# Kernel tuning notes

Hardware: AMD Instinct MI355X
Metric: run time of the kernel (lower is better)

Reference implementation:

```python
import jax, jax.numpy as jnp
import numpy as np

D_MODEL = 1024
NUM_HEADS = 16
HEAD_DIM = D_MODEL // NUM_HEADS


def setup_inputs() -> dict:
    key = jax.random.key(0)
    ks = jax.random.split(key, 9)
    s = 1.0 / np.sqrt(D_MODEL)
    x = jax.random.normal(ks[0], (2, 2048, D_MODEL), dtype=jnp.float32)
    Wq = jax.random.normal(ks[1], (D_MODEL, D_MODEL), dtype=jnp.float32) * s
    bq = jnp.zeros((D_MODEL,), dtype=jnp.float32)
    Wk = jax.random.normal(ks[2], (D_MODEL, D_MODEL), dtype=jnp.float32) * s
    bk = jnp.zeros((D_MODEL,), dtype=jnp.float32)
    Wv = jax.random.normal(ks[3], (D_MODEL, D_MODEL), dtype=jnp.float32) * s
    bv = jnp.zeros((D_MODEL,), dtype=jnp.float32)
    Wo = jax.random.normal(ks[4], (D_MODEL, D_MODEL), dtype=jnp.float32) * s
    bo = jnp.zeros((D_MODEL,), dtype=jnp.float32)
    return {"x": x, "Wq": Wq, "bq": bq, "Wk": Wk, "bk": bk,
            "Wv": Wv, "bv": bv, "Wo": Wo, "bo": bo}


def reference(x, Wq, bq, Wk, bk, Wv, bv, Wo, bo):
    B, S, D = x.shape
    H, Hd = NUM_HEADS, HEAD_DIM
    scale = 1.0 / np.sqrt(Hd)

    def split_heads(t):  # [B,S,D] -> [B,H,S,Hd]
        return t.reshape(B, S, H, Hd).transpose(0, 2, 1, 3)

    q = split_heads(x @ Wq + bq)
    k = split_heads(x @ Wk + bk)
    v = split_heads(x @ Wv + bv)

    scores = jnp.einsum('bhqd,bhkd->bhqk', q, k) * scale
    scores = scores - jnp.max(scores, axis=-1, keepdims=True)
    attn = jax.nn.softmax(scores, axis=-1)
    attended = jnp.einsum('bhqk,bhkd->bhqd', attn, v)
    attended = attended.transpose(0, 2, 1, 3).reshape(B, S, D)
    return attended @ Wo + bo
```

## Files before the change

### kernel.cpp

```cpp
#include <hip/hip_runtime.h>
#include <hip/hip_bf16.h>

typedef __bf16 bf16_t;
typedef __bf16 bf16x8 __attribute__((ext_vector_type(8)));
typedef __bf16 bf16x4 __attribute__((ext_vector_type(4)));
typedef float floatx4 __attribute__((ext_vector_type(4)));
typedef short short4v __attribute__((ext_vector_type(4)));

#define D_MODEL 1024
#define SEQ     2048
#define BATCH   2
#define NHEAD   16
#define HDIM    64
#define MTOT    (BATCH * SEQ)
#define LROWS   (32 * 2048)
#define OPS     (32 * 64 * 2048)

#define QSCALE  0.18033688011112042f

union PBu { bf16x4 b; short4v s; };

__device__ __forceinline__ void async_copy16(const bf16_t* g, bf16_t* l) {
    __builtin_amdgcn_global_load_lds(
        (const __attribute__((address_space(1))) void*)g,
        (__attribute__((address_space(3))) void*)l, 16, 0, 0);
}

__global__ void cvt_f32_bf16(const float* __restrict__ x, bf16_t* __restrict__ y, int n) {
    int i = (blockIdx.x * 256 + threadIdx.x) * 4;
    if (i < n) {
        const float4 v = *(const float4*)(x + i);
        bf16x4 o = { (bf16_t)v.x, (bf16_t)v.y, (bf16_t)v.z, (bf16_t)v.w };
        *(bf16x4*)(y + i) = o;
    }
}

__global__ void transpose_w4(
    const float* __restrict__ W0, const float* __restrict__ W1,
    const float* __restrict__ W2, const float* __restrict__ W3,
    bf16_t* __restrict__ T0, bf16_t* __restrict__ T1,
    bf16_t* __restrict__ T2, bf16_t* __restrict__ T3)
{
    __shared__ float tile[32][33];
    const int z = blockIdx.z;
    const float* W = (z == 0) ? W0 : (z == 1) ? W1 : (z == 2) ? W2 : W3;
    bf16_t*     Wt = (z == 0) ? T0 : (z == 1) ? T1 : (z == 2) ? T2 : T3;
    const int tx = threadIdx.x, ty = threadIdx.y;
    const int k0 = blockIdx.y * 32, n0 = blockIdx.x * 32;
#pragma unroll
    for (int j = 0; j < 32; j += 8)
        tile[ty + j][tx] = W[(size_t)(k0 + ty + j) * D_MODEL + n0 + tx];
    __syncthreads();
#pragma unroll
    for (int j = 0; j < 32; j += 8)
        Wt[(size_t)(n0 + ty + j) * D_MODEL + k0 + tx] = (bf16_t)tile[tx][ty + j];
}

__device__ __forceinline__ void gemm_mainloop(
    const bf16_t* __restrict__ A, const bf16_t* __restrict__ Bt,
    int m0, int n0, bf16_t* As, bf16_t* Bs, floatx4 acc[4][4])
{
    const int tid  = threadIdx.x;
    const int lane = tid & 63;
    const int wid  = tid >> 6;
    const int quad = lane >> 4;
    const int col  = lane & 15;
    const int wm   = (wid >> 1) * 64;
    const int wn   = (wid & 1) * 64;
    const int srow = tid >> 3;
    const int scc  = ((tid & 7) ^ (srow & 7)) * 8;
    const int xorc = col & 7;

    const bf16_t* Ag = A  + (size_t)(m0 + srow) * D_MODEL + scc;
    const bf16_t* Bg = Bt + (size_t)(n0 + srow) * D_MODEL + scc;
    bf16_t* Al = As + tid * 8;
    bf16_t* Bl = Bs + tid * 8;

    for (int kb = 0; kb < D_MODEL; kb += 64) {
#pragma unroll
        for (int p = 0; p < 4; ++p) {
            async_copy16(Ag + kb + p * (32 * D_MODEL), Al + p * 2048);
            async_copy16(Bg + kb + p * (32 * D_MODEL), Bl + p * 2048);
        }
        __syncthreads();
#pragma unroll
        for (int kh = 0; kh < 2; ++kh) {
            bf16x8 af[4], bfr[4];
#pragma unroll
            for (int i = 0; i < 4; ++i)
                af[i] = *(const bf16x8*)(As + (wm + i * 16 + col) * 64 + (((kh * 4 + quad) ^ xorc) * 8));
#pragma unroll
            for (int j = 0; j < 4; ++j)
                bfr[j] = *(const bf16x8*)(Bs + (wn + j * 16 + col) * 64 + (((kh * 4 + quad) ^ xorc) * 8));
#pragma unroll
            for (int i = 0; i < 4; ++i)
#pragma unroll
                for (int j = 0; j < 4; ++j)
                    acc[i][j] = __builtin_amdgcn_mfma_f32_16x16x32_bf16(af[i], bfr[j], acc[i][j], 0, 0, 0);
        }
        __syncthreads();
    }
}

__global__ __launch_bounds__(256, 2) void gemm_qkv(
    const bf16_t* __restrict__ xb,
    const bf16_t* __restrict__ Wtq, const bf16_t* __restrict__ Wtk, const bf16_t* __restrict__ Wtv,
    const float* __restrict__ bq, const float* __restrict__ bk, const float* __restrict__ bv,
    bf16_t* __restrict__ Q, bf16_t* __restrict__ Kh, bf16_t* __restrict__ Vt)
{
    __shared__ bf16_t As[128 * 64];
    __shared__ bf16_t Bs[128 * 64];
    const int z = blockIdx.z;
    const bf16_t* Bt   = (z == 0) ? Wtq : (z == 1) ? Wtk : Wtv;
    const float*  bias = (z == 0) ? bq  : (z == 1) ? bk  : bv;
    bf16_t*       O    = (z == 0) ? Q   : (z == 1) ? Kh  : Vt;
    const float   qs   = (z == 0) ? QSCALE : 1.0f;
    const int m0 = blockIdx.y * 128;
    const int n0 = blockIdx.x * 128;

    floatx4 acc[4][4];
#pragma unroll
    for (int i = 0; i < 4; ++i)
#pragma unroll
        for (int j = 0; j < 4; ++j)
            acc[i][j] = (floatx4){0.f, 0.f, 0.f, 0.f};

    gemm_mainloop(xb, Bt, m0, n0, As, Bs, acc);

    const int tid  = threadIdx.x;
    const int lane = tid & 63;
    const int wid  = tid >> 6;
    const int quad = lane >> 4;
    const int col  = lane & 15;
    const int wm   = (wid >> 1) * 64;
    const int wn   = (wid & 1) * 64;

    if (z == 2) {
#pragma unroll
        for (int i = 0; i < 4; ++i) {
#pragma unroll
            for (int j = 0; j < 4; ++j) {
                const int n = n0 + wn + j * 16 + col;
                const float bb = bias[n];
                const int mb = m0 + wm + i * 16 + quad * 4;
                const size_t bhb = (size_t)((mb >> 11) * NHEAD + (n >> 6)) * (SEQ * HDIM);
                bf16x4 pk = { (bf16_t)(acc[i][j][0] + bb), (bf16_t)(acc[i][j][1] + bb),
                              (bf16_t)(acc[i][j][2] + bb), (bf16_t)(acc[i][j][3] + bb) };
                *(bf16x4*)(O + bhb + (size_t)(n & 63) * SEQ + (mb & 2047)) = pk;
            }
        }
    } else {
#pragma unroll
        for (int i = 0; i < 4; ++i) {
#pragma unroll
            for (int j = 0; j < 4; ++j) {
                const int n = n0 + wn + j * 16 + col;
                const float bb = bias[n];
#pragma unroll
                for (int r = 0; r < 4; ++r) {
                    const int m = m0 + wm + i * 16 + quad * 4 + r;
                    const float v = (acc[i][j][r] + bb) * qs;
                    const size_t bhb = (size_t)((m >> 11) * NHEAD + (n >> 6)) * (SEQ * HDIM);
                    O[bhb + (size_t)(m & 2047) * HDIM + (n & 63)] = (bf16_t)v;
                }
            }
        }
    }
}

__global__ __launch_bounds__(256, 3) void attn_kernel(
    const bf16_t* __restrict__ Q, const bf16_t* __restrict__ K,
    const bf16_t* __restrict__ Vt, float* __restrict__ Opart, float* __restrict__ lpart)
{
    __shared__ bf16_t Ks[64 * 64];
    __shared__ bf16_t Vs[64 * 64];

    const int tid  = threadIdx.x;
    const int lane = tid & 63;
    const int wid  = tid >> 6;
    const int quad = lane >> 4;
    const int col  = lane & 15;
    const int xorc = col & 7;
    const int bh   = blockIdx.y;
    const int sp   = blockIdx.z;
    const int q0   = blockIdx.x * 128;
    const int srow = tid >> 3;
    const int scc  = ((tid & 7) ^ (srow & 7)) * 8;

    const bf16_t* Qb = Q  + (size_t)bh * (SEQ * HDIM);
    const bf16_t* Kb = K  + (size_t)bh * (SEQ * HDIM);
    const bf16_t* Vb = Vt + (size_t)bh * (SEQ * HDIM);

    bf16x8 qf[2][2];
#pragma unroll
    for (int st = 0; st < 2; ++st) {
        const int qrow = q0 + wid * 32 + st * 16 + col;
        qf[st][0] = *(const bf16x8*)(Qb + (size_t)qrow * HDIM + quad * 8);
        qf[st][1] = *(const bf16x8*)(Qb + (size_t)qrow * HDIM + 32 + quad * 8);
    }

    floatx4 o_acc[2][4];
    float lsum[2] = {0.f, 0.f};
#pragma unroll
    for (int st = 0; st < 2; ++st)
#pragma unroll
        for (int dt = 0; dt < 4; ++dt)
            o_acc[st][dt] = (floatx4){0.f, 0.f, 0.f, 0.f};

    const bf16_t* Kg = Kb + (size_t)(sp * 1024 + srow) * HDIM + scc;
    const bf16_t* Vg = Vb + (size_t)srow * SEQ + sp * 1024 + scc;
    bf16_t* KsL = Ks + tid * 8;
    bf16_t* VsL = Vs + tid * 8;

    for (int it = 0; it < 16; ++it) {
        const int ko = it * 64;
        async_copy16(Kg + (size_t)ko * HDIM, KsL);
        async_copy16(Kg + (size_t)(ko + 32) * HDIM, KsL + 2048);
        async_copy16(Vg + ko, VsL);
        async_copy16(Vg + (size_t)32 * SEQ + ko, VsL + 2048);
        __syncthreads();

        bf16x8 kf[4][2];
#pragma unroll
        for (int t = 0; t < 4; ++t) {
            kf[t][0] = *(const bf16x8*)(Ks + (t * 16 + col) * 64 + ((quad ^ xorc) * 8));
            kf[t][1] = *(const bf16x8*)(Ks + (t * 16 + col) * 64 + (((4 + quad) ^ xorc) * 8));
        }
        short4v vfr[4][4];
#pragma unroll
        for (int dt = 0; dt < 4; ++dt)
#pragma unroll
            for (int t = 0; t < 4; ++t) {
                const int sch = t * 2 + (quad >> 1);
                vfr[dt][t] = *(const short4v*)(Vs + (dt * 16 + col) * 64 + ((sch ^ xorc) * 8) + (quad & 1) * 4);
            }

#pragma unroll
        for (int st = 0; st < 2; ++st) {
            floatx4 s_acc[4];
            short4v pb[4];
#pragma unroll
            for (int t = 0; t < 4; ++t) {
                s_acc[t] = (floatx4){0.f, 0.f, 0.f, 0.f};
                s_acc[t] = __builtin_amdgcn_mfma_f32_16x16x32_bf16(kf[t][0], qf[st][0], s_acc[t], 0, 0, 0);
                s_acc[t] = __builtin_amdgcn_mfma_f32_16x16x32_bf16(kf[t][1], qf[st][1], s_acc[t], 0, 0, 0);
            }
#pragma unroll
            for (int t = 0; t < 4; ++t) {
                const float p0 = exp2f(s_acc[t][0]);
                const float p1 = exp2f(s_acc[t][1]);
                const float p2 = exp2f(s_acc[t][2]);
                const float p3 = exp2f(s_acc[t][3]);
                lsum[st] += (p0 + p1) + (p2 + p3);
                PBu u;
                u.b = (bf16x4){ (bf16_t)p0, (bf16_t)p1, (bf16_t)p2, (bf16_t)p3 };
                pb[t] = u.s;
            }
#pragma unroll
            for (int dt = 0; dt < 4; ++dt)
#pragma unroll
                for (int t = 0; t < 4; ++t)
                    o_acc[st][dt] = __builtin_amdgcn_mfma_f32_16x16x16bf16_1k(vfr[dt][t], pb[t], o_acc[st][dt], 0, 0, 0);
        }
        __syncthreads();
    }

#pragma unroll
    for (int st = 0; st < 2; ++st) {
        lsum[st] += __shfl_xor(lsum[st], 16, 64);
        lsum[st] += __shfl_xor(lsum[st], 32, 64);
    }

    const size_t osp = (size_t)sp * OPS + (size_t)bh * 64 * 2048;
#pragma unroll
    for (int st = 0; st < 2; ++st) {
        const int q = q0 + wid * 32 + st * 16 + col;
#pragma unroll
        for (int dt = 0; dt < 4; ++dt)
#pragma unroll
            for (int r = 0; r < 4; ++r) {
                const int d = dt * 16 + quad * 4 + r;
                Opart[osp + (size_t)d * 2048 + q] = o_acc[st][dt][r];
            }
        if (lane < 16)
            lpart[(size_t)sp * LROWS + (size_t)bh * 2048 + q0 + wid * 32 + st * 16 + lane] = lsum[st];
    }
}

__global__ __launch_bounds__(256) void attn_combine(
    const float* __restrict__ Op, const float* __restrict__ lp, bf16_t* __restrict__ A2)
{
    __shared__ float Linv[64];
    __shared__ bf16_t T[64 * 72];
    const int tid = threadIdx.x;
    const int qb  = blockIdx.x * 64;
    const int bh  = blockIdx.y;
    const int b   = bh >> 4, h = bh & 15;

    if (tid < 64)
        Linv[tid] = 1.0f / (lp[(size_t)bh * 2048 + qb + tid] + lp[LROWS + (size_t)bh * 2048 + qb + tid]);
    __syncthreads();

    const int d  = tid >> 2;
    const int qo = (tid & 3) * 16;
    const size_t base = ((size_t)bh * 64 + d) * 2048 + qb + qo;
#pragma unroll
    for (int i = 0; i < 16; i += 4) {
        const float4 a = *(const float4*)(Op + base + i);
        const float4 c = *(const float4*)(Op + OPS + base + i);
        T[(qo + i + 0) * 72 + d] = (bf16_t)((a.x + c.x) * Linv[qo + i + 0]);
        T[(qo + i + 1) * 72 + d] = (bf16_t)((a.y + c.y) * Linv[qo + i + 1]);
        T[(qo + i + 2) * 72 + d] = (bf16_t)((a.z + c.z) * Linv[qo + i + 2]);
        T[(qo + i + 3) * 72 + d] = (bf16_t)((a.w + c.w) * Linv[qo + i + 3]);
    }
    __syncthreads();

    const int q  = tid >> 2;
    const int dd = (tid & 3) * 16;
    const bf16x8 o0 = *(const bf16x8*)(T + q * 72 + dd);
    const bf16x8 o1 = *(const bf16x8*)(T + q * 72 + dd + 8);
    bf16_t* dst = A2 + ((size_t)(b * 2048 + qb + q)) * D_MODEL + h * 64 + dd;
    *(bf16x8*)(dst) = o0;
    *(bf16x8*)(dst + 8) = o1;
}

__global__ __launch_bounds__(256, 2) void gemm_proj(
    const bf16_t* __restrict__ A2, const bf16_t* __restrict__ Wto,
    const float* __restrict__ bo, float* __restrict__ out)
{
    __shared__ bf16_t As[128 * 64];
    __shared__ bf16_t Bs[128 * 64];
    const int m0 = blockIdx.y * 128;
    const int n0 = blockIdx.x * 128;

    floatx4 acc[4][4];
#pragma unroll
    for (int i = 0; i < 4; ++i)
#pragma unroll
        for (int j = 0; j < 4; ++j)
            acc[i][j] = (floatx4){0.f, 0.f, 0.f, 0.f};

    gemm_mainloop(A2, Wto, m0, n0, As, Bs, acc);

    const int tid  = threadIdx.x;
    const int lane = tid & 63;
    const int wid  = tid >> 6;
    const int quad = lane >> 4;
    const int col  = lane & 15;
    const int wm   = (wid >> 1) * 64;
    const int wn   = (wid & 1) * 64;

#pragma unroll
    for (int i = 0; i < 4; ++i) {
#pragma unroll
        for (int j = 0; j < 4; ++j) {
            const int n = n0 + wn + j * 16 + col;
            const float bb = bo[n];
#pragma unroll
            for (int r = 0; r < 4; ++r) {
                const int m = m0 + wm + i * 16 + quad * 4 + r;
                out[(size_t)m * D_MODEL + n] = acc[i][j][r] + bb;
            }
        }
    }
}

extern "C" void kernel_launch(void* const* d_in, const int* in_sizes, int n_in,
                              void* d_out, int out_size, void* d_ws, size_t ws_size,
                              hipStream_t stream) {
    const float* x  = (const float*)d_in[0];
    const float* Wq = (const float*)d_in[1];
    const float* bq = (const float*)d_in[2];
    const float* Wk = (const float*)d_in[3];
    const float* bk = (const float*)d_in[4];
    const float* Wv = (const float*)d_in[5];
    const float* bv = (const float*)d_in[6];
    const float* Wo = (const float*)d_in[7];
    const float* bo = (const float*)d_in[8];
    float* out = (float*)d_out;

    const size_t MB = 1ull << 20;
    char* ws = (char*)d_ws;
    bf16_t* Q     = (bf16_t*)(ws + 0 * MB);
    bf16_t* Kh    = (bf16_t*)(ws + 8 * MB);
    bf16_t* Vt    = (bf16_t*)(ws + 16 * MB);
    bf16_t* A2    = (bf16_t*)(ws + 24 * MB);
    bf16_t* xb    = (bf16_t*)(ws + 32 * MB);
    float*  lpart = (float*)(ws + 32 * MB);
    bf16_t* Wtq   = (bf16_t*)(ws + 40 * MB);
    bf16_t* Wtk   = (bf16_t*)(ws + 42 * MB);
    bf16_t* Wtv   = (bf16_t*)(ws + 44 * MB);
    bf16_t* Wto   = (bf16_t*)(ws + 46 * MB);
    float*  Opart = (float*)(ws + 48 * MB);

    const int nx = MTOT * D_MODEL;
    cvt_f32_bf16<<<nx / (256 * 4), 256, 0, stream>>>(x, xb, nx);

    transpose_w4<<<dim3(D_MODEL / 32, D_MODEL / 32, 4), dim3(32, 8), 0, stream>>>(
        Wq, Wk, Wv, Wo, Wtq, Wtk, Wtv, Wto);

    gemm_qkv<<<dim3(D_MODEL / 128, MTOT / 128, 3), 256, 0, stream>>>(
        xb, Wtq, Wtk, Wtv, bq, bk, bv, Q, Kh, Vt);

    attn_kernel<<<dim3(SEQ / 128, BATCH * NHEAD, 2), 256, 0, stream>>>(
        Q, Kh, Vt, Opart, lpart);

    attn_combine<<<dim3(SEQ / 64, BATCH * NHEAD), 256, 0, stream>>>(Opart, lpart, A2);

    gemm_proj<<<dim3(D_MODEL / 128, MTOT / 128), 256, 0, stream>>>(A2, Wto, bo, out);
}
```

Baseline: 210.4 us.

## Enlarge attention KV tile to 128, shrink proj GEMM M tile, raise occupancy

The attention kernel now stages 128 keys and values per iteration instead of 64. That halves the number of loop iterations and barriers, at the cost of twice the LDS per block, while the occupancy hint rises to 4. The output projection GEMM moves to 64x128 tiles with its own inlined main loop, doubling the grid size so more blocks cover the CUs. Occupancy hints on the QKV and projection GEMMs are also raised to 3, which may force register pressure or spills.

```diff
diff --git a/kernel.cpp b/kernel.cpp
--- a/kernel.cpp
+++ b/kernel.cpp
@@ -102,7 +102,7 @@
     }
 }
 
-__global__ __launch_bounds__(256, 2) void gemm_qkv(
+__global__ __launch_bounds__(256, 3) void gemm_qkv(
     const bf16_t* __restrict__ xb,
     const bf16_t* __restrict__ Wtq, const bf16_t* __restrict__ Wtk, const bf16_t* __restrict__ Wtv,
     const float* __restrict__ bq, const float* __restrict__ bk, const float* __restrict__ bv,
@@ -168,12 +168,12 @@
     }
 }
 
-__global__ __launch_bounds__(256, 3) void attn_kernel(
+__global__ __launch_bounds__(256, 4) void attn_kernel(
     const bf16_t* __restrict__ Q, const bf16_t* __restrict__ K,
     const bf16_t* __restrict__ Vt, float* __restrict__ Opart, float* __restrict__ lpart)
 {
-    __shared__ bf16_t Ks[64 * 64];
-    __shared__ bf16_t Vs[64 * 64];
+    __shared__ bf16_t Ks[128 * 64];
+    __shared__ bf16_t Vs[64 * 128];
 
     const int tid  = threadIdx.x;
     const int lane = tid & 63;
@@ -184,8 +184,6 @@
     const int bh   = blockIdx.y;
     const int sp   = blockIdx.z;
     const int q0   = blockIdx.x * 128;
-    const int srow = tid >> 3;
-    const int scc  = ((tid & 7) ^ (srow & 7)) * 8;
 
     const bf16_t* Qb = Q  + (size_t)bh * (SEQ * HDIM);
     const bf16_t* Kb = K  + (size_t)bh * (SEQ * HDIM);
@@ -207,60 +205,68 @@
         for (int dt = 0; dt < 4; ++dt)
             o_acc[st][dt] = (floatx4){0.f, 0.f, 0.f, 0.f};
 
-    const bf16_t* Kg = Kb + (size_t)(sp * 1024 + srow) * HDIM + scc;
-    const bf16_t* Vg = Vb + (size_t)srow * SEQ + sp * 1024 + scc;
+    const int krow = tid >> 3;
+    const int sccK = ((tid & 7) ^ (krow & 7)) * 8;
+    const int vrow = tid >> 4;
+    const int sccV = ((tid & 15) ^ (vrow & 7)) * 8;
+    const bf16_t* Kg = Kb + (size_t)(sp * 1024 + krow) * HDIM + sccK;
+    const bf16_t* Vg = Vb + (size_t)vrow * SEQ + sp * 1024 + sccV;
     bf16_t* KsL = Ks + tid * 8;
     bf16_t* VsL = Vs + tid * 8;
 
-    for (int it = 0; it < 16; ++it) {
-        const int ko = it * 64;
-        async_copy16(Kg + (size_t)ko * HDIM, KsL);
-        async_copy16(Kg + (size_t)(ko + 32) * HDIM, KsL + 2048);
-        async_copy16(Vg + ko, VsL);
-        async_copy16(Vg + (size_t)32 * SEQ + ko, VsL + 2048);
-        __syncthreads();
-
-        bf16x8 kf[4][2];
-#pragma unroll
-        for (int t = 0; t < 4; ++t) {
-            kf[t][0] = *(const bf16x8*)(Ks + (t * 16 + col) * 64 + ((quad ^ xorc) * 8));
-            kf[t][1] = *(const bf16x8*)(Ks + (t * 16 + col) * 64 + (((4 + quad) ^ xorc) * 8));
-        }
-        short4v vfr[4][4];
-#pragma unroll
-        for (int dt = 0; dt < 4; ++dt)
+    for (int it = 0; it < 8; ++it) {
+        const int ko = it * 128;
+#pragma unroll
+        for (int p = 0; p < 4; ++p) {
+            async_copy16(Kg + (size_t)(ko + p * 32) * HDIM, KsL + p * 2048);
+            async_copy16(Vg + ko + (size_t)(p * 16) * SEQ, VsL + p * 2048);
+        }
+        __syncthreads();
+
+#pragma unroll
+        for (int kh = 0; kh < 2; ++kh) {
+            bf16x8 kf[4][2];
 #pragma unroll
             for (int t = 0; t < 4; ++t) {
-                const int sch = t * 2 + (quad >> 1);
-                vfr[dt][t] = *(const short4v*)(Vs + (dt * 16 + col) * 64 + ((sch ^ xorc) * 8) + (quad & 1) * 4);
-            }
-
-#pragma unroll
-        for (int st = 0; st < 2; ++st) {
-            floatx4 s_acc[4];
-            short4v pb[4];
-#pragma unroll
-            for (int t = 0; t < 4; ++t) {
-                s_acc[t] = (floatx4){0.f, 0.f, 0.f, 0.f};
-                s_acc[t] = __builtin_amdgcn_mfma_f32_16x16x32_bf16(kf[t][0], qf[st][0], s_acc[t], 0, 0, 0);
-                s_acc[t] = __builtin_amdgcn_mfma_f32_16x16x32_bf16(kf[t][1], qf[st][1], s_acc[t], 0, 0, 0);
-            }
-#pragma unroll
-            for (int t = 0; t < 4; ++t) {
-                const float p0 = exp2f(s_acc[t][0]);
-                const float p1 = exp2f(s_acc[t][1]);
-                const float p2 = exp2f(s_acc[t][2]);
-                const float p3 = exp2f(s_acc[t][3]);
-                lsum[st] += (p0 + p1) + (p2 + p3);
-                PBu u;
-                u.b = (bf16x4){ (bf16_t)p0, (bf16_t)p1, (bf16_t)p2, (bf16_t)p3 };
-                pb[t] = u.s;
-            }
+                kf[t][0] = *(const bf16x8*)(Ks + (kh * 64 + t * 16 + col) * 64 + ((quad ^ xorc) * 8));
+                kf[t][1] = *(const bf16x8*)(Ks + (kh * 64 + t * 16 + col) * 64 + (((4 + quad) ^ xorc) * 8));
+            }
+            short4v vfr[4][4];
 #pragma unroll
             for (int dt = 0; dt < 4; ++dt)
 #pragma unroll
-                for (int t = 0; t < 4; ++t)
-                    o_acc[st][dt] = __builtin_amdgcn_mfma_f32_16x16x16bf16_1k(vfr[dt][t], pb[t], o_acc[st][dt], 0, 0, 0);
+                for (int t = 0; t < 4; ++t) {
+                    const int sch = kh * 8 + t * 2 + (quad >> 1);
+                    vfr[dt][t] = *(const short4v*)(Vs + (dt * 16 + col) * 128 + ((sch ^ xorc) * 8) + (quad & 1) * 4);
+                }
+
+#pragma unroll
+            for (int st = 0; st < 2; ++st) {
+                floatx4 s_acc[4];
+                short4v pb[4];
+#pragma unroll
+                for (int t = 0; t < 4; ++t) {
+                    s_acc[t] = (floatx4){0.f, 0.f, 0.f, 0.f};
+                    s_acc[t] = __builtin_amdgcn_mfma_f32_16x16x32_bf16(kf[t][0], qf[st][0], s_acc[t], 0, 0, 0);
+                    s_acc[t] = __builtin_amdgcn_mfma_f32_16x16x32_bf16(kf[t][1], qf[st][1], s_acc[t], 0, 0, 0);
+                }
+#pragma unroll
+                for (int t = 0; t < 4; ++t) {
+                    const float p0 = exp2f(s_acc[t][0]);
+                    const float p1 = exp2f(s_acc[t][1]);
+                    const float p2 = exp2f(s_acc[t][2]);
+                    const float p3 = exp2f(s_acc[t][3]);
+                    lsum[st] += (p0 + p1) + (p2 + p3);
+                    PBu u;
+                    u.b = (bf16x4){ (bf16_t)p0, (bf16_t)p1, (bf16_t)p2, (bf16_t)p3 };
+                    pb[t] = u.s;
+                }
+#pragma unroll
+                for (int dt = 0; dt < 4; ++dt)
+#pragma unroll
+                    for (int t = 0; t < 4; ++t)
+                        o_acc[st][dt] = __builtin_amdgcn_mfma_f32_16x16x16bf16_1k(vfr[dt][t], pb[t], o_acc[st][dt], 0, 0, 0);
+            }
         }
         __syncthreads();
     }
@@ -324,34 +330,66 @@
     *(bf16x8*)(dst + 8) = o1;
 }
 
-__global__ __launch_bounds__(256, 2) void gemm_proj(
+__global__ __launch_bounds__(256, 3) void gemm_proj(
     const bf16_t* __restrict__ A2, const bf16_t* __restrict__ Wto,
     const float* __restrict__ bo, float* __restrict__ out)
 {
-    __shared__ bf16_t As[128 * 64];
+    __shared__ bf16_t As[64 * 64];
     __shared__ bf16_t Bs[128 * 64];
-    const int m0 = blockIdx.y * 128;
+    const int m0 = blockIdx.y * 64;
     const int n0 = blockIdx.x * 128;
-
-    floatx4 acc[4][4];
-#pragma unroll
-    for (int i = 0; i < 4; ++i)
-#pragma unroll
-        for (int j = 0; j < 4; ++j)
-            acc[i][j] = (floatx4){0.f, 0.f, 0.f, 0.f};
-
-    gemm_mainloop(A2, Wto, m0, n0, As, Bs, acc);
 
     const int tid  = threadIdx.x;
     const int lane = tid & 63;
     const int wid  = tid >> 6;
     const int quad = lane >> 4;
     const int col  = lane & 15;
-    const int wm   = (wid >> 1) * 64;
+    const int wm   = (wid >> 1) * 32;
     const int wn   = (wid & 1) * 64;
-
-#pragma unroll
-    for (int i = 0; i < 4; ++i) {
+    const int srow = tid >> 3;
+    const int scc  = ((tid & 7) ^ (srow & 7)) * 8;
+    const int xorc = col & 7;
+
+    floatx4 acc[2][4];
+#pragma unroll
+    for (int i = 0; i < 2; ++i)
+#pragma unroll
+        for (int j = 0; j < 4; ++j)
+            acc[i][j] = (floatx4){0.f, 0.f, 0.f, 0.f};
+
+    const bf16_t* Ag = A2  + (size_t)(m0 + srow) * D_MODEL + scc;
+    const bf16_t* Bg = Wto + (size_t)(n0 + srow) * D_MODEL + scc;
+    bf16_t* Al = As + tid * 8;
+    bf16_t* Bl = Bs + tid * 8;
+
+    for (int kb = 0; kb < D_MODEL; kb += 64) {
+#pragma unroll
+        for (int p = 0; p < 2; ++p)
+            async_copy16(Ag + kb + p * (32 * D_MODEL), Al + p * 2048);
+#pragma unroll
+        for (int p = 0; p < 4; ++p)
+            async_copy16(Bg + kb + p * (32 * D_MODEL), Bl + p * 2048);
+        __syncthreads();
+#pragma unroll
+        for (int kh = 0; kh < 2; ++kh) {
+            bf16x8 af[2], bfr[4];
+#pragma unroll
+            for (int i = 0; i < 2; ++i)
+                af[i] = *(const bf16x8*)(As + (wm + i * 16 + col) * 64 + (((kh * 4 + quad) ^ xorc) * 8));
+#pragma unroll
+            for (int j = 0; j < 4; ++j)
+                bfr[j] = *(const bf16x8*)(Bs + (wn + j * 16 + col) * 64 + (((kh * 4 + quad) ^ xorc) * 8));
+#pragma unroll
+            for (int i = 0; i < 2; ++i)
+#pragma unroll
+                for (int j = 0; j < 4; ++j)
+                    acc[i][j] = __builtin_amdgcn_mfma_f32_16x16x32_bf16(af[i], bfr[j], acc[i][j], 0, 0, 0);
+        }
+        __syncthreads();
+    }
+
+#pragma unroll
+    for (int i = 0; i < 2; ++i) {
 #pragma unroll
         for (int j = 0; j < 4; ++j) {
             const int n = n0 + wn + j * 16 + col;
@@ -407,5 +445,5 @@
 
     attn_combine<<<dim3(SEQ / 64, BATCH * NHEAD), 256, 0, stream>>>(Opart, lpart, A2);
 
-    gemm_proj<<<dim3(D_MODEL / 128, MTOT / 128), 256, 0, stream>>>(A2, Wto, bo, out);
-}
+    gemm_proj<<<dim3(D_MODEL / 128, MTOT / 64), 256, 0, stream>>>(A2, Wto, bo, out);
+}
```

New measurement: 237.1 us. 1.13x slower.

## Drop split-K attention and combine kernel; normalize in attention epilogue

Applied to the files above, without the earlier changes.

The attention kernel no longer splits the key range in two and writes fp32 partial outputs and row sums for a separate combine kernel. Each block now handles 64 queries over the full 2048 keys, normalizes in registers and writes bf16 output directly into the projection input layout. Blocks are remapped so that all queries of one head are spread across the block index. This removes a kernel launch and the fp32 partial round trip, at the cost of half the per-block Q reuse of K/V tiles. The output projection GEMM moves to a 64x128 tile with higher occupancy bounds, QKV occupancy is raised, and exp2f is replaced with the hardware exp2 intrinsic.

```diff
diff --git a/kernel.cpp b/kernel.cpp
--- a/kernel.cpp
+++ b/kernel.cpp
@@ -13,8 +13,6 @@
 #define NHEAD   16
 #define HDIM    64
 #define MTOT    (BATCH * SEQ)
-#define LROWS   (32 * 2048)
-#define OPS     (32 * 64 * 2048)
 
 #define QSCALE  0.18033688011112042f
 
@@ -102,7 +100,7 @@
     }
 }
 
-__global__ __launch_bounds__(256, 2) void gemm_qkv(
+__global__ __launch_bounds__(256, 3) void gemm_qkv(
     const bf16_t* __restrict__ xb,
     const bf16_t* __restrict__ Wtq, const bf16_t* __restrict__ Wtk, const bf16_t* __restrict__ Wtv,
     const float* __restrict__ bq, const float* __restrict__ bk, const float* __restrict__ bv,
@@ -168,9 +166,9 @@
     }
 }
 
-__global__ __launch_bounds__(256, 3) void attn_kernel(
+__global__ __launch_bounds__(256, 4) void attn_kernel(
     const bf16_t* __restrict__ Q, const bf16_t* __restrict__ K,
-    const bf16_t* __restrict__ Vt, float* __restrict__ Opart, float* __restrict__ lpart)
+    const bf16_t* __restrict__ Vt, bf16_t* __restrict__ A2)
 {
     __shared__ bf16_t Ks[64 * 64];
     __shared__ bf16_t Vs[64 * 64];
@@ -181,38 +179,35 @@
     const int quad = lane >> 4;
     const int col  = lane & 15;
     const int xorc = col & 7;
-    const int bh   = blockIdx.y;
-    const int sp   = blockIdx.z;
-    const int q0   = blockIdx.x * 128;
-    const int srow = tid >> 3;
-    const int scc  = ((tid & 7) ^ (srow & 7)) * 8;
+
+    const int blk = blockIdx.x;
+    const int idx = blk >> 3;
+    const int bh  = (blk & 7) * 4 + (idx >> 5);
+    const int q0  = (idx & 31) * 64;
+    const int b   = bh >> 4, h = bh & 15;
 
     const bf16_t* Qb = Q  + (size_t)bh * (SEQ * HDIM);
     const bf16_t* Kb = K  + (size_t)bh * (SEQ * HDIM);
     const bf16_t* Vb = Vt + (size_t)bh * (SEQ * HDIM);
 
-    bf16x8 qf[2][2];
-#pragma unroll
-    for (int st = 0; st < 2; ++st) {
-        const int qrow = q0 + wid * 32 + st * 16 + col;
-        qf[st][0] = *(const bf16x8*)(Qb + (size_t)qrow * HDIM + quad * 8);
-        qf[st][1] = *(const bf16x8*)(Qb + (size_t)qrow * HDIM + 32 + quad * 8);
-    }
-
-    floatx4 o_acc[2][4];
-    float lsum[2] = {0.f, 0.f};
-#pragma unroll
-    for (int st = 0; st < 2; ++st)
-#pragma unroll
-        for (int dt = 0; dt < 4; ++dt)
-            o_acc[st][dt] = (floatx4){0.f, 0.f, 0.f, 0.f};
-
-    const bf16_t* Kg = Kb + (size_t)(sp * 1024 + srow) * HDIM + scc;
-    const bf16_t* Vg = Vb + (size_t)srow * SEQ + sp * 1024 + scc;
+    const int qrow = q0 + wid * 16 + col;
+    bf16x8 qf0 = *(const bf16x8*)(Qb + (size_t)qrow * HDIM + quad * 8);
+    bf16x8 qf1 = *(const bf16x8*)(Qb + (size_t)qrow * HDIM + 32 + quad * 8);
+
+    floatx4 o_acc[4];
+    float lsum = 0.f;
+#pragma unroll
+    for (int dt = 0; dt < 4; ++dt)
+        o_acc[dt] = (floatx4){0.f, 0.f, 0.f, 0.f};
+
+    const int srow = tid >> 3;
+    const int scc  = ((tid & 7) ^ (srow & 7)) * 8;
+    const bf16_t* Kg = Kb + (size_t)srow * HDIM + scc;
+    const bf16_t* Vg = Vb + (size_t)srow * SEQ + scc;
     bf16_t* KsL = Ks + tid * 8;
     bf16_t* VsL = Vs + tid * 8;
 
-    for (int it = 0; it < 16; ++it) {
+    for (int it = 0; it < 32; ++it) {
         const int ko = it * 64;
         async_copy16(Kg + (size_t)ko * HDIM, KsL);
         async_copy16(Kg + (size_t)(ko + 32) * HDIM, KsL + 2048);
@@ -235,123 +230,106 @@
                 vfr[dt][t] = *(const short4v*)(Vs + (dt * 16 + col) * 64 + ((sch ^ xorc) * 8) + (quad & 1) * 4);
             }
 
-#pragma unroll
-        for (int st = 0; st < 2; ++st) {
-            floatx4 s_acc[4];
-            short4v pb[4];
-#pragma unroll
-            for (int t = 0; t < 4; ++t) {
-                s_acc[t] = (floatx4){0.f, 0.f, 0.f, 0.f};
-                s_acc[t] = __builtin_amdgcn_mfma_f32_16x16x32_bf16(kf[t][0], qf[st][0], s_acc[t], 0, 0, 0);
-                s_acc[t] = __builtin_amdgcn_mfma_f32_16x16x32_bf16(kf[t][1], qf[st][1], s_acc[t], 0, 0, 0);
-            }
-#pragma unroll
-            for (int t = 0; t < 4; ++t) {
-                const float p0 = exp2f(s_acc[t][0]);
-                const float p1 = exp2f(s_acc[t][1]);
-                const float p2 = exp2f(s_acc[t][2]);
-                const float p3 = exp2f(s_acc[t][3]);
-                lsum[st] += (p0 + p1) + (p2 + p3);
-                PBu u;
-                u.b = (bf16x4){ (bf16_t)p0, (bf16_t)p1, (bf16_t)p2, (bf16_t)p3 };
-                pb[t] = u.s;
-            }
-#pragma unroll
-            for (int dt = 0; dt < 4; ++dt)
-#pragma unroll
-                for (int t = 0; t < 4; ++t)
-                    o_acc[st][dt] = __builtin_amdgcn_mfma_f32_16x16x16bf16_1k(vfr[dt][t], pb[t], o_acc[st][dt], 0, 0, 0);
-        }
-        __syncthreads();
-    }
-
-#pragma unroll
-    for (int st = 0; st < 2; ++st) {
-        lsum[st] += __shfl_xor(lsum[st], 16, 64);
-        lsum[st] += __shfl_xor(lsum[st], 32, 64);
-    }
-
-    const size_t osp = (size_t)sp * OPS + (size_t)bh * 64 * 2048;
-#pragma unroll
-    for (int st = 0; st < 2; ++st) {
-        const int q = q0 + wid * 32 + st * 16 + col;
+        floatx4 s_acc[4];
+        short4v pb[4];
+#pragma unroll
+        for (int t = 0; t < 4; ++t) {
+            s_acc[t] = (floatx4){0.f, 0.f, 0.f, 0.f};
+            s_acc[t] = __builtin_amdgcn_mfma_f32_16x16x32_bf16(kf[t][0], qf0, s_acc[t], 0, 0, 0);
+            s_acc[t] = __builtin_amdgcn_mfma_f32_16x16x32_bf16(kf[t][1], qf1, s_acc[t], 0, 0, 0);
+        }
+#pragma unroll
+        for (int t = 0; t < 4; ++t) {
+            const float p0 = __builtin_amdgcn_exp2f(s_acc[t][0]);
+            const float p1 = __builtin_amdgcn_exp2f(s_acc[t][1]);
+            const float p2 = __builtin_amdgcn_exp2f(s_acc[t][2]);
+            const float p3 = __builtin_amdgcn_exp2f(s_acc[t][3]);
+            lsum += (p0 + p1) + (p2 + p3);
+            PBu u;
+            u.b = (bf16x4){ (bf16_t)p0, (bf16_t)p1, (bf16_t)p2, (bf16_t)p3 };
+            pb[t] = u.s;
+        }
 #pragma unroll
         for (int dt = 0; dt < 4; ++dt)
 #pragma unroll
-            for (int r = 0; r < 4; ++r) {
-                const int d = dt * 16 + quad * 4 + r;
-                Opart[osp + (size_t)d * 2048 + q] = o_acc[st][dt][r];
-            }
-        if (lane < 16)
-            lpart[(size_t)sp * LROWS + (size_t)bh * 2048 + q0 + wid * 32 + st * 16 + lane] = lsum[st];
-    }
-}
-
-__global__ __launch_bounds__(256) void attn_combine(
-    const float* __restrict__ Op, const float* __restrict__ lp, bf16_t* __restrict__ A2)
-{
-    __shared__ float Linv[64];
-    __shared__ bf16_t T[64 * 72];
-    const int tid = threadIdx.x;
-    const int qb  = blockIdx.x * 64;
-    const int bh  = blockIdx.y;
-    const int b   = bh >> 4, h = bh & 15;
-
-    if (tid < 64)
-        Linv[tid] = 1.0f / (lp[(size_t)bh * 2048 + qb + tid] + lp[LROWS + (size_t)bh * 2048 + qb + tid]);
-    __syncthreads();
-
-    const int d  = tid >> 2;
-    const int qo = (tid & 3) * 16;
-    const size_t base = ((size_t)bh * 64 + d) * 2048 + qb + qo;
-#pragma unroll
-    for (int i = 0; i < 16; i += 4) {
-        const float4 a = *(const float4*)(Op + base + i);
-        const float4 c = *(const float4*)(Op + OPS + base + i);
-        T[(qo + i + 0) * 72 + d] = (bf16_t)((a.x + c.x) * Linv[qo + i + 0]);
-        T[(qo + i + 1) * 72 + d] = (bf16_t)((a.y + c.y) * Linv[qo + i + 1]);
-        T[(qo + i + 2) * 72 + d] = (bf16_t)((a.z + c.z) * Linv[qo + i + 2]);
-        T[(qo + i + 3) * 72 + d] = (bf16_t)((a.w + c.w) * Linv[qo + i + 3]);
-    }
-    __syncthreads();
-
-    const int q  = tid >> 2;
-    const int dd = (tid & 3) * 16;
-    const bf16x8 o0 = *(const bf16x8*)(T + q * 72 + dd);
-    const bf16x8 o1 = *(const bf16x8*)(T + q * 72 + dd + 8);
-    bf16_t* dst = A2 + ((size_t)(b * 2048 + qb + q)) * D_MODEL + h * 64 + dd;
-    *(bf16x8*)(dst) = o0;
-    *(bf16x8*)(dst + 8) = o1;
-}
-
-__global__ __launch_bounds__(256, 2) void gemm_proj(
+            for (int t = 0; t < 4; ++t)
+                o_acc[dt] = __builtin_amdgcn_mfma_f32_16x16x16bf16_1k(vfr[dt][t], pb[t], o_acc[dt], 0, 0, 0);
+        __syncthreads();
+    }
+
+    lsum += __shfl_xor(lsum, 16, 64);
+    lsum += __shfl_xor(lsum, 32, 64);
+    const float inv = 1.0f / lsum;
+
+    bf16_t* dst = A2 + ((size_t)(b * SEQ + qrow)) * D_MODEL + h * HDIM + quad * 4;
+#pragma unroll
+    for (int dt = 0; dt < 4; ++dt) {
+        bf16x4 pk = { (bf16_t)(o_acc[dt][0] * inv), (bf16_t)(o_acc[dt][1] * inv),
+                      (bf16_t)(o_acc[dt][2] * inv), (bf16_t)(o_acc[dt][3] * inv) };
+        *(bf16x4*)(dst + dt * 16) = pk;
+    }
+}
+
+__global__ __launch_bounds__(256, 3) void gemm_proj(
     const bf16_t* __restrict__ A2, const bf16_t* __restrict__ Wto,
     const float* __restrict__ bo, float* __restrict__ out)
 {
-    __shared__ bf16_t As[128 * 64];
+    __shared__ bf16_t As[64 * 64];
     __shared__ bf16_t Bs[128 * 64];
-    const int m0 = blockIdx.y * 128;
+    const int m0 = blockIdx.y * 64;
     const int n0 = blockIdx.x * 128;
-
-    floatx4 acc[4][4];
-#pragma unroll
-    for (int i = 0; i < 4; ++i)
-#pragma unroll
-        for (int j = 0; j < 4; ++j)
-            acc[i][j] = (floatx4){0.f, 0.f, 0.f, 0.f};
-
-    gemm_mainloop(A2, Wto, m0, n0, As, Bs, acc);
 
     const int tid  = threadIdx.x;
     const int lane = tid & 63;
     const int wid  = tid >> 6;
     const int quad = lane >> 4;
     const int col  = lane & 15;
-    const int wm   = (wid >> 1) * 64;
+    const int wm   = (wid >> 1) * 32;
     const int wn   = (wid & 1) * 64;
-
-#pragma unroll
-    for (int i = 0; i < 4; ++i) {
+    const int srow = tid >> 3;
+    const int scc  = ((tid & 7) ^ (srow & 7)) * 8;
+    const int xorc = col & 7;
+
+    floatx4 acc[2][4];
+#pragma unroll
+    for (int i = 0; i < 2; ++i)
+#pragma unroll
+        for (int j = 0; j < 4; ++j)
+            acc[i][j] = (floatx4){0.f, 0.f, 0.f, 0.f};
+
+    const bf16_t* Ag = A2  + (size_t)(m0 + srow) * D_MODEL + scc;
+    const bf16_t* Bg = Wto + (size_t)(n0 + srow) * D_MODEL + scc;
+    bf16_t* Al = As + tid * 8;
+    bf16_t* Bl = Bs + tid * 8;
+
+    for (int kb = 0; kb < D_MODEL; kb += 64) {
+#pragma unroll
+        for (int p = 0; p < 2; ++p)
+            async_copy16(Ag + kb + p * (32 * D_MODEL), Al + p * 2048);
+#pragma unroll
+        for (int p = 0; p < 4; ++p)
+            async_copy16(Bg + kb + p * (32 * D_MODEL), Bl + p * 2048);
+        __syncthreads();
+#pragma unroll
+        for (int kh = 0; kh < 2; ++kh) {
+            bf16x8 af[2], bfr[4];
+#pragma unroll
+            for (int i = 0; i < 2; ++i)
+                af[i] = *(const bf16x8*)(As + (wm + i * 16 + col) * 64 + (((kh * 4 + quad) ^ xorc) * 8));
+#pragma unroll
+            for (int j = 0; j < 4; ++j)
+                bfr[j] = *(const bf16x8*)(Bs + (wn + j * 16 + col) * 64 + (((kh * 4 + quad) ^ xorc) * 8));
+#pragma unroll
+            for (int i = 0; i < 2; ++i)
+#pragma unroll
+                for (int j = 0; j < 4; ++j)
+                    acc[i][j] = __builtin_amdgcn_mfma_f32_16x16x32_bf16(af[i], bfr[j], acc[i][j], 0, 0, 0);
+        }
+        __syncthreads();
+    }
+
+#pragma unroll
+    for (int i = 0; i < 2; ++i) {
 #pragma unroll
         for (int j = 0; j < 4; ++j) {
             const int n = n0 + wn + j * 16 + col;
@@ -386,12 +364,10 @@
     bf16_t* Vt    = (bf16_t*)(ws + 16 * MB);
     bf16_t* A2    = (bf16_t*)(ws + 24 * MB);
     bf16_t* xb    = (bf16_t*)(ws + 32 * MB);
-    float*  lpart = (float*)(ws + 32 * MB);
     bf16_t* Wtq   = (bf16_t*)(ws + 40 * MB);
     bf16_t* Wtk   = (bf16_t*)(ws + 42 * MB);
     bf16_t* Wtv   = (bf16_t*)(ws + 44 * MB);
     bf16_t* Wto   = (bf16_t*)(ws + 46 * MB);
-    float*  Opart = (float*)(ws + 48 * MB);
 
     const int nx = MTOT * D_MODEL;
     cvt_f32_bf16<<<nx / (256 * 4), 256, 0, stream>>>(x, xb, nx);
@@ -402,10 +378,7 @@
     gemm_qkv<<<dim3(D_MODEL / 128, MTOT / 128, 3), 256, 0, stream>>>(
         xb, Wtq, Wtk, Wtv, bq, bk, bv, Q, Kh, Vt);
 
-    attn_kernel<<<dim3(SEQ / 128, BATCH * NHEAD, 2), 256, 0, stream>>>(
-        Q, Kh, Vt, Opart, lpart);
-
-    attn_combine<<<dim3(SEQ / 64, BATCH * NHEAD), 256, 0, stream>>>(Opart, lpart, A2);
-
-    gemm_proj<<<dim3(D_MODEL / 128, MTOT / 128), 256, 0, stream>>>(A2, Wto, bo, out);
-}
+    attn_kernel<<<dim3(1024), 256, 0, stream>>>(Q, Kh, Vt, A2);
+
+    gemm_proj<<<dim3(D_MODEL / 128, MTOT / 64), 256, 0, stream>>>(A2, Wto, bo, out);
+}
```

Result: faster. 188.7 us (-10.3%).
